# Kernel optimization log

Hardware: AMD Instinct MI355X
Metric: run time of the kernel (lower is better)

Reference implementation:

```python
import jax, jax.numpy as jnp
import numpy as np

# ProbLog program semantics, closed-form:
# Grid 2x2, cell index = 2*X + Y: 0=(0,0), 1=(0,1), 2=(1,0), 3=(1,1).
# Actions (query order): 0=stay, 1=up, 2=down, 3=left, 4=right.
# transition/5 only defines clauses for stay/up/down (plus west/east which never
# unify with left/right), so left/right can never produce 'unsafe'.
# unsafe :- pacman(X,Y), action(A), transition(X,Y,A,X1,Y1), ghost(X1,Y1).
# evidence(safe) conditions the action query: P(a|safe) = p_a(a)*safe(a)/sum.

def _build_T():
    T = np.zeros((5, 4, 4), dtype=np.float32)  # [action, pac_cell, ghost_cell]
    for c in range(4):
        T[0, c, c] = 1.0  # stay
    # up: (x,y)->(x,y+1): cell0->1, cell2->3 (y=1 cells move off-grid -> no ghost)
    T[1, 0, 1] = 1.0
    T[1, 2, 3] = 1.0
    # down: (x,y)->(x,y-1): cell1->0, cell3->2
    T[2, 1, 0] = 1.0
    T[2, 3, 2] = 1.0
    # left/right: no transition clauses -> always safe
    return T

_T = _build_T()


def setup_inputs() -> dict:
    key = jax.random.key(0)
    ks = jax.random.split(key, 4)
    B, H = 16384, 2048
    s = 1.0 / np.sqrt(H)
    return {
        "x": jax.random.normal(ks[0], (B, H), dtype=jnp.float32),
        "Wg": jax.random.normal(ks[1], (H, 4), dtype=jnp.float32) * s,
        "bg": jnp.zeros((4,), dtype=jnp.float32),
        "Wp": jax.random.normal(ks[2], (H, 4), dtype=jnp.float32) * s,
        "bp": jnp.zeros((4,), dtype=jnp.float32),
        "Wa": jax.random.normal(ks[3], (H, 5), dtype=jnp.float32) * s,
        "ba": jnp.zeros((5,), dtype=jnp.float32),
    }


def reference(x, Wg, bg, Wp, bp, Wa, ba):
    ghost = jax.nn.softmax(x @ Wg + bg, axis=-1)   # [B,4]
    pacman = jax.nn.softmax(x @ Wp + bp, axis=-1)  # [B,4]
    base = jax.nn.softmax(x @ Wa + ba, axis=-1)    # [B,5]
    T = jnp.asarray(_T)                            # [5,4,4]
    # P(unsafe | action=a) = sum_c pac[c] * ghost[target(c,a)]
    unsafe = jnp.einsum('bc,acd,bd->ba', pacman, T, ghost)  # [B,5]
    joint = base * (1.0 - unsafe)                  # P(action=a, safe)
    return joint / jnp.sum(joint, axis=-1, keepdims=True)   # P(action=a | safe)
```

## Files before the change

kernel.cpp:

```cpp
#include <hip/hip_runtime.h>
#include <hip/hip_fp16.h>


__global__ __launch_bounds__(256, 2)
void dpl_safe_policy_kernel(const float* __restrict__ x,
                            const float* __restrict__ Wg, const float* __restrict__ bg,
                            const float* __restrict__ Wp, const float* __restrict__ bp,
                            const float* __restrict__ Wa, const float* __restrict__ ba,
                            float* __restrict__ out)
{
    __shared__ __half wlds[13 * 2048];
    __shared__ float4 xt[4][2][72];

    const int tid = threadIdx.x;

    for (int idx = tid; idx < 13 * 2048; idx += 256) {
        const int j = idx >> 11, h = idx & 2047;
        float v;
        if (j < 4)      v = Wg[h * 4 + j];
        else if (j < 8) v = Wp[h * 4 + (j - 4)];
        else            v = Wa[h * 5 + (j - 8)];
        wlds[idx] = __float2half(v);
    }
    __syncthreads();

    const int w  = tid >> 6;
    const int l  = tid & 63;
    const int r8 = l & 7;
    const int p  = l >> 3;
    const int rowbase = blockIdx.x * 32 + w * 8;

    const float4* xg = (const float4*)x;
    const long gbase = (long)(rowbase + p) * 512 + r8;

    float4* tw = &xt[w][0][0];
    const int wr_off = p * 9 + r8;
    const int rd_off = r8 * 9 + p;

    float4 x0 = xg[gbase];
    tw[wr_off] = x0;
    float4 xn0 = xg[gbase + 8];
    float4 xn1 = xg[gbase + 16];
    float4 xn2 = xg[gbase + 24];

    float acc[13];
    #pragma unroll
    for (int j = 0; j < 13; ++j) acc[j] = 0.f;

    const __half2* w2 = (const __half2*)wlds;

    #pragma unroll 4
    for (int c = 0; c < 64; ++c) {
        const int buf = c & 1;
        if (c + 1 < 64) tw[(buf ^ 1) * 72 + wr_off] = xn0;
        xn0 = xn1; xn1 = xn2;
        if (c + 4 < 64) xn2 = xg[gbase + (c + 4) * 8];
        const float4 xv = tw[buf * 72 + rd_off];
        const int wb = c * 16 + p * 2;
        #pragma unroll
        for (int j = 0; j < 13; ++j) {
            const __half2 ha = w2[j * 1024 + wb];
            const __half2 hb = w2[j * 1024 + wb + 1];
            const float2 fa = __half22float2(ha);
            const float2 fb = __half22float2(hb);
            acc[j] += xv.x * fa.x + xv.y * fa.y + xv.z * fb.x + xv.w * fb.y;
        }
    }

    #pragma unroll
    for (int j = 0; j < 13; ++j) {
        acc[j] += __shfl_xor(acc[j], 8,  64);
        acc[j] += __shfl_xor(acc[j], 16, 64);
        acc[j] += __shfl_xor(acc[j], 32, 64);
    }

    const float g0 = acc[0] + bg[0], g1 = acc[1] + bg[1], g2 = acc[2] + bg[2], g3 = acc[3] + bg[3];
    const float q0 = acc[4] + bp[0], q1 = acc[5] + bp[1], q2 = acc[6] + bp[2], q3 = acc[7] + bp[3];
    const float a0 = acc[8] + ba[0], a1 = acc[9] + ba[1], a2 = acc[10] + ba[2],
                a3 = acc[11] + ba[3], a4 = acc[12] + ba[4];

    float m, s, inv;
    m = fmaxf(fmaxf(g0, g1), fmaxf(g2, g3));
    const float eg0 = __expf(g0 - m), eg1 = __expf(g1 - m), eg2 = __expf(g2 - m), eg3 = __expf(g3 - m);
    s = eg0 + eg1 + eg2 + eg3; inv = 1.f / s;
    const float G0 = eg0 * inv, G1 = eg1 * inv, G2 = eg2 * inv, G3 = eg3 * inv;

    m = fmaxf(fmaxf(q0, q1), fmaxf(q2, q3));
    const float ep0 = __expf(q0 - m), ep1 = __expf(q1 - m), ep2 = __expf(q2 - m), ep3 = __expf(q3 - m);
    s = ep0 + ep1 + ep2 + ep3; inv = 1.f / s;
    const float P0 = ep0 * inv, P1 = ep1 * inv, P2 = ep2 * inv, P3 = ep3 * inv;

    m = fmaxf(fmaxf(fmaxf(a0, a1), fmaxf(a2, a3)), a4);
    const float ea0 = __expf(a0 - m), ea1 = __expf(a1 - m), ea2 = __expf(a2 - m),
                ea3 = __expf(a3 - m), ea4 = __expf(a4 - m);
    s = ea0 + ea1 + ea2 + ea3 + ea4; inv = 1.f / s;
    const float A0 = ea0 * inv, A1 = ea1 * inv, A2 = ea2 * inv, A3 = ea3 * inv, A4 = ea4 * inv;

    const float u0 = P0 * G0 + P1 * G1 + P2 * G2 + P3 * G3;
    const float u1 = P0 * G1 + P2 * G3;
    const float u2 = P1 * G0 + P3 * G2;

    const float j0 = A0 * (1.f - u0), j1 = A1 * (1.f - u1), j2 = A2 * (1.f - u2),
                j3 = A3, j4 = A4;
    const float isd = 1.f / (j0 + j1 + j2 + j3 + j4);

    const int row = rowbase + r8;
    const float ov = (p == 0) ? j0 : (p == 1) ? j1 : (p == 2) ? j2 : (p == 3) ? j3 : j4;
    if (p < 5) out[row * 5 + p] = ov * isd;
}

extern "C" void kernel_launch(void* const* d_in, const int* in_sizes, int n_in,
                              void* d_out, int out_size, void* d_ws, size_t ws_size,
                              hipStream_t stream) {
    const float* x  = (const float*)d_in[0];
    const float* Wg = (const float*)d_in[1];
    const float* bg = (const float*)d_in[2];
    const float* Wp = (const float*)d_in[3];
    const float* bp = (const float*)d_in[4];
    const float* Wa = (const float*)d_in[5];
    const float* ba = (const float*)d_in[6];
    float* out = (float*)d_out;

    const int B = in_sizes[0] / 2048;
    const int grid = B / 32;
    dpl_safe_policy_kernel<<<grid, 256, 0, stream>>>(x, Wg, bg, Wp, bp, Wa, ba, out);
}
```

Baseline: 224.3 us.

## Restructure GEMV to two rows per lane with packed fp16 dot2 and no LDS transpose

Each lane now processes two rows over 16 H-slices, so every LDS weight load is reused for two rows. The LDS transpose buffer for x is removed in favour of direct coalesced float4 loads with a two-step register prefetch. x is converted to packed fp16 and accumulated with v_dot2 instructions. Weight staging into LDS now uses vectorized float4 reads. This cuts LDS traffic and FMA count, at the cost of quantizing x to fp16 with round-toward-zero, which could reduce accuracy, plus more accumulator registers.

```diff
diff --git a/kernel.cpp b/kernel.cpp
--- a/kernel.cpp
+++ b/kernel.cpp
@@ -1,6 +1,9 @@
 #include <hip/hip_runtime.h>
 #include <hip/hip_fp16.h>
 
+
+typedef __fp16 h2_t __attribute__((ext_vector_type(2)));
+typedef __fp16 h4_t __attribute__((ext_vector_type(4)));
 
 __global__ __launch_bounds__(256, 2)
 void dpl_safe_policy_kernel(const float* __restrict__ x,
@@ -9,104 +12,135 @@
                             const float* __restrict__ Wa, const float* __restrict__ ba,
                             float* __restrict__ out)
 {
-    __shared__ __half wlds[13 * 2048];
-    __shared__ float4 xt[4][2][72];
+    __shared__ __align__(16) __fp16 wlds[13 * 2048];
 
     const int tid = threadIdx.x;
 
-    for (int idx = tid; idx < 13 * 2048; idx += 256) {
-        const int j = idx >> 11, h = idx & 2047;
-        float v;
-        if (j < 4)      v = Wg[h * 4 + j];
-        else if (j < 8) v = Wp[h * 4 + (j - 4)];
-        else            v = Wa[h * 5 + (j - 8)];
-        wlds[idx] = __float2half(v);
+    const float4* Wg4 = (const float4*)Wg;
+    const float4* Wp4 = (const float4*)Wp;
+    for (int h = tid; h < 2048; h += 256) {
+        float4 g = Wg4[h];
+        wlds[0 * 2048 + h] = (__fp16)g.x;
+        wlds[1 * 2048 + h] = (__fp16)g.y;
+        wlds[2 * 2048 + h] = (__fp16)g.z;
+        wlds[3 * 2048 + h] = (__fp16)g.w;
+        float4 p = Wp4[h];
+        wlds[4 * 2048 + h] = (__fp16)p.x;
+        wlds[5 * 2048 + h] = (__fp16)p.y;
+        wlds[6 * 2048 + h] = (__fp16)p.z;
+        wlds[7 * 2048 + h] = (__fp16)p.w;
+        #pragma unroll
+        for (int j = 0; j < 5; ++j)
+            wlds[(8 + j) * 2048 + h] = (__fp16)Wa[h * 5 + j];
     }
     __syncthreads();
 
     const int w  = tid >> 6;
     const int l  = tid & 63;
-    const int r8 = l & 7;
-    const int p  = l >> 3;
+    const int hs = l & 15;
+    const int rg = l >> 4;
     const int rowbase = blockIdx.x * 32 + w * 8;
+    const int row0 = rowbase + rg * 2;
 
     const float4* xg = (const float4*)x;
-    const long gbase = (long)(rowbase + p) * 512 + r8;
+    const long b0 = (long)row0 * 512 + hs;
+    const long b1 = b0 + 512;
 
-    float4* tw = &xt[w][0][0];
-    const int wr_off = p * 9 + r8;
-    const int rd_off = r8 * 9 + p;
+    const h4_t* w4 = (const h4_t*)wlds;
 
-    float4 x0 = xg[gbase];
-    tw[wr_off] = x0;
-    float4 xn0 = xg[gbase + 8];
-    float4 xn1 = xg[gbase + 16];
-    float4 xn2 = xg[gbase + 24];
+    float acc0[13], acc1[13];
+    #pragma unroll
+    for (int j = 0; j < 13; ++j) { acc0[j] = 0.f; acc1[j] = 0.f; }
 
-    float acc[13];
-    #pragma unroll
-    for (int j = 0; j < 13; ++j) acc[j] = 0.f;
+    float4 c00 = xg[b0],      c10 = xg[b1];
+    float4 c01 = xg[b0 + 16], c11 = xg[b1 + 16];
 
-    const __half2* w2 = (const __half2*)wlds;
-
-    #pragma unroll 4
-    for (int c = 0; c < 64; ++c) {
-        const int buf = c & 1;
-        if (c + 1 < 64) tw[(buf ^ 1) * 72 + wr_off] = xn0;
-        xn0 = xn1; xn1 = xn2;
-        if (c + 4 < 64) xn2 = xg[gbase + (c + 4) * 8];
-        const float4 xv = tw[buf * 72 + rd_off];
-        const int wb = c * 16 + p * 2;
+    #pragma unroll 2
+    for (int c = 0; c < 32; ++c) {
+        const float4 xv0 = c00, xv1 = c10;
+        c00 = c01; c10 = c11;
+        if (c + 2 < 32) {
+            c01 = xg[b0 + (c + 2) * 16];
+            c11 = xg[b1 + (c + 2) * 16];
+        }
+        const h2_t xl0 = __builtin_amdgcn_cvt_pkrtz(xv0.x, xv0.y);
+        const h2_t xh0 = __builtin_amdgcn_cvt_pkrtz(xv0.z, xv0.w);
+        const h2_t xl1 = __builtin_amdgcn_cvt_pkrtz(xv1.x, xv1.y);
+        const h2_t xh1 = __builtin_amdgcn_cvt_pkrtz(xv1.z, xv1.w);
+        const int wb = c * 16 + hs;
         #pragma unroll
         for (int j = 0; j < 13; ++j) {
-            const __half2 ha = w2[j * 1024 + wb];
-            const __half2 hb = w2[j * 1024 + wb + 1];
-            const float2 fa = __half22float2(ha);
-            const float2 fb = __half22float2(hb);
-            acc[j] += xv.x * fa.x + xv.y * fa.y + xv.z * fb.x + xv.w * fb.y;
+            const h4_t wv = w4[j * 512 + wb];
+            const h2_t wlo = __builtin_shufflevector(wv, wv, 0, 1);
+            const h2_t whi = __builtin_shufflevector(wv, wv, 2, 3);
+#if __has_builtin(__builtin_amdgcn_fdot2)
+            acc0[j] = __builtin_amdgcn_fdot2(xl0, wlo, acc0[j], false);
+            acc0[j] = __builtin_amdgcn_fdot2(xh0, whi, acc0[j], false);
+            acc1[j] = __builtin_amdgcn_fdot2(xl1, wlo, acc1[j], false);
+            acc1[j] = __builtin_amdgcn_fdot2(xh1, whi, acc1[j], false);
+#else
+            acc0[j] += (float)xl0.x * (float)wlo.x + (float)xl0.y * (float)wlo.y
+                     + (float)xh0.x * (float)whi.x + (float)xh0.y * (float)whi.y;
+            acc1[j] += (float)xl1.x * (float)wlo.x + (float)xl1.y * (float)wlo.y
+                     + (float)xh1.x * (float)whi.x + (float)xh1.y * (float)whi.y;
+#endif
         }
     }
 
     #pragma unroll
     for (int j = 0; j < 13; ++j) {
-        acc[j] += __shfl_xor(acc[j], 8,  64);
-        acc[j] += __shfl_xor(acc[j], 16, 64);
-        acc[j] += __shfl_xor(acc[j], 32, 64);
+        acc0[j] += __shfl_xor(acc0[j], 1, 64);
+        acc0[j] += __shfl_xor(acc0[j], 2, 64);
+        acc0[j] += __shfl_xor(acc0[j], 4, 64);
+        acc0[j] += __shfl_xor(acc0[j], 8, 64);
+        acc1[j] += __shfl_xor(acc1[j], 1, 64);
+        acc1[j] += __shfl_xor(acc1[j], 2, 64);
+        acc1[j] += __shfl_xor(acc1[j], 4, 64);
+        acc1[j] += __shfl_xor(acc1[j], 8, 64);
     }
 
-    const float g0 = acc[0] + bg[0], g1 = acc[1] + bg[1], g2 = acc[2] + bg[2], g3 = acc[3] + bg[3];
-    const float q0 = acc[4] + bp[0], q1 = acc[5] + bp[1], q2 = acc[6] + bp[2], q3 = acc[7] + bp[3];
-    const float a0 = acc[8] + ba[0], a1 = acc[9] + ba[1], a2 = acc[10] + ba[2],
-                a3 = acc[11] + ba[3], a4 = acc[12] + ba[4];
+    const float vbg0 = bg[0], vbg1 = bg[1], vbg2 = bg[2], vbg3 = bg[3];
+    const float vbp0 = bp[0], vbp1 = bp[1], vbp2 = bp[2], vbp3 = bp[3];
+    const float vba0 = ba[0], vba1 = ba[1], vba2 = ba[2], vba3 = ba[3], vba4 = ba[4];
 
-    float m, s, inv;
-    m = fmaxf(fmaxf(g0, g1), fmaxf(g2, g3));
-    const float eg0 = __expf(g0 - m), eg1 = __expf(g1 - m), eg2 = __expf(g2 - m), eg3 = __expf(g3 - m);
-    s = eg0 + eg1 + eg2 + eg3; inv = 1.f / s;
-    const float G0 = eg0 * inv, G1 = eg1 * inv, G2 = eg2 * inv, G3 = eg3 * inv;
+    #pragma unroll
+    for (int r = 0; r < 2; ++r) {
+        const float* acc = r ? acc1 : acc0;
+        const float g0 = acc[0] + vbg0, g1 = acc[1] + vbg1, g2 = acc[2] + vbg2, g3 = acc[3] + vbg3;
+        const float q0 = acc[4] + vbp0, q1 = acc[5] + vbp1, q2 = acc[6] + vbp2, q3 = acc[7] + vbp3;
+        const float a0 = acc[8] + vba0, a1 = acc[9] + vba1, a2 = acc[10] + vba2,
+                    a3 = acc[11] + vba3, a4 = acc[12] + vba4;
 
-    m = fmaxf(fmaxf(q0, q1), fmaxf(q2, q3));
-    const float ep0 = __expf(q0 - m), ep1 = __expf(q1 - m), ep2 = __expf(q2 - m), ep3 = __expf(q3 - m);
-    s = ep0 + ep1 + ep2 + ep3; inv = 1.f / s;
-    const float P0 = ep0 * inv, P1 = ep1 * inv, P2 = ep2 * inv, P3 = ep3 * inv;
+        float m, s, inv;
+        m = fmaxf(fmaxf(g0, g1), fmaxf(g2, g3));
+        const float eg0 = __expf(g0 - m), eg1 = __expf(g1 - m), eg2 = __expf(g2 - m), eg3 = __expf(g3 - m);
+        s = eg0 + eg1 + eg2 + eg3; inv = 1.f / s;
+        const float G0 = eg0 * inv, G1 = eg1 * inv, G2 = eg2 * inv, G3 = eg3 * inv;
 
-    m = fmaxf(fmaxf(fmaxf(a0, a1), fmaxf(a2, a3)), a4);
-    const float ea0 = __expf(a0 - m), ea1 = __expf(a1 - m), ea2 = __expf(a2 - m),
-                ea3 = __expf(a3 - m), ea4 = __expf(a4 - m);
-    s = ea0 + ea1 + ea2 + ea3 + ea4; inv = 1.f / s;
-    const float A0 = ea0 * inv, A1 = ea1 * inv, A2 = ea2 * inv, A3 = ea3 * inv, A4 = ea4 * inv;
+        m = fmaxf(fmaxf(q0, q1), fmaxf(q2, q3));
+        const float ep0 = __expf(q0 - m), ep1 = __expf(q1 - m), ep2 = __expf(q2 - m), ep3 = __expf(q3 - m);
+        s = ep0 + ep1 + ep2 + ep3; inv = 1.f / s;
+        const float P0 = ep0 * inv, P1 = ep1 * inv, P2 = ep2 * inv, P3 = ep3 * inv;
 
-    const float u0 = P0 * G0 + P1 * G1 + P2 * G2 + P3 * G3;
-    const float u1 = P0 * G1 + P2 * G3;
-    const float u2 = P1 * G0 + P3 * G2;
+        m = fmaxf(fmaxf(fmaxf(a0, a1), fmaxf(a2, a3)), a4);
+        const float ea0 = __expf(a0 - m), ea1 = __expf(a1 - m), ea2 = __expf(a2 - m),
+                    ea3 = __expf(a3 - m), ea4 = __expf(a4 - m);
+        s = ea0 + ea1 + ea2 + ea3 + ea4; inv = 1.f / s;
+        const float A0 = ea0 * inv, A1 = ea1 * inv, A2 = ea2 * inv, A3 = ea3 * inv, A4 = ea4 * inv;
 
-    const float j0 = A0 * (1.f - u0), j1 = A1 * (1.f - u1), j2 = A2 * (1.f - u2),
-                j3 = A3, j4 = A4;
-    const float isd = 1.f / (j0 + j1 + j2 + j3 + j4);
+        const float u0 = P0 * G0 + P1 * G1 + P2 * G2 + P3 * G3;
+        const float u1 = P0 * G1 + P2 * G3;
+        const float u2 = P1 * G0 + P3 * G2;
 
-    const int row = rowbase + r8;
-    const float ov = (p == 0) ? j0 : (p == 1) ? j1 : (p == 2) ? j2 : (p == 3) ? j3 : j4;
-    if (p < 5) out[row * 5 + p] = ov * isd;
+        const float j0 = A0 * (1.f - u0), j1 = A1 * (1.f - u1), j2 = A2 * (1.f - u2),
+                    j3 = A3, j4 = A4;
+        const float isd = 1.f / (j0 + j1 + j2 + j3 + j4);
+
+        if (hs < 5) {
+            const float ov = (hs == 0) ? j0 : (hs == 1) ? j1 : (hs == 2) ? j2 : (hs == 3) ? j3 : j4;
+            out[(row0 + r) * 5 + hs] = ov * isd;
+        }
+    }
 }
 
 extern "C" void kernel_launch(void* const* d_in, const int* in_sizes, int n_in,
```

Result: faster. 210.2 us (-6.3%).

## Replace scalar FMA dot products with fp16 MFMA using prepacked weight fragments

Applied to the files above, without the earlier changes.

Adds a small pre-kernel that converts the concatenated weights to fp16 and packs them into MFMA B-fragment order in workspace. The main kernel converts x tiles to fp16 in registers and runs 16x16x32 MFMAs, with each block's K dimension split across wave pairs and the partial sums combined through shared memory. This removes the per-block LDS weight staging and the scalar FMA loop. It costs an extra kernel launch, rounds x to fp16, and uses hardcoded grid sizes.

```diff
diff --git a/kernel.cpp b/kernel.cpp
--- a/kernel.cpp
+++ b/kernel.cpp
@@ -1,112 +1,129 @@
 #include <hip/hip_runtime.h>
-#include <hip/hip_fp16.h>
 
 
+typedef __fp16 h2_t __attribute__((ext_vector_type(2)));
+typedef __fp16 h4_t __attribute__((ext_vector_type(4)));
+typedef __fp16 h8_t __attribute__((ext_vector_type(8)));
+typedef float f32x4 __attribute__((ext_vector_type(4)));
+
+__global__ void pack_bfrag(const float* __restrict__ Wg,
+                           const float* __restrict__ Wp,
+                           const float* __restrict__ Wa,
+                           h8_t* __restrict__ bfrag)
+{
+    const int t = blockIdx.x * 256 + threadIdx.x;
+    const int iter = t >> 6, lane = t & 63;
+    const int n = lane & 15, kg = lane >> 4;
+    h8_t v;
+    #pragma unroll
+    for (int j = 0; j < 8; ++j) {
+        const int k = iter * 32 + kg * 8 + j;
+        float f;
+        if (n < 4)       f = Wg[k * 4 + n];
+        else if (n < 8)  f = Wp[k * 4 + (n - 4)];
+        else if (n < 13) f = Wa[k * 5 + (n - 8)];
+        else             f = 0.f;
+        v[j] = (__fp16)f;
+    }
+    bfrag[t] = v;
+}
+
 __global__ __launch_bounds__(256, 2)
-void dpl_safe_policy_kernel(const float* __restrict__ x,
-                            const float* __restrict__ Wg, const float* __restrict__ bg,
-                            const float* __restrict__ Wp, const float* __restrict__ bp,
-                            const float* __restrict__ Wa, const float* __restrict__ ba,
-                            float* __restrict__ out)
+void gemm_mfma(const float* __restrict__ x,
+               const h8_t* __restrict__ bfrag,
+               const float* __restrict__ bg, const float* __restrict__ bp,
+               const float* __restrict__ ba, float* __restrict__ out)
 {
-    __shared__ __half wlds[13 * 2048];
-    __shared__ float4 xt[4][2][72];
+    __shared__ float dt[2][2][16][17];
 
     const int tid = threadIdx.x;
-
-    for (int idx = tid; idx < 13 * 2048; idx += 256) {
-        const int j = idx >> 11, h = idx & 2047;
-        float v;
-        if (j < 4)      v = Wg[h * 4 + j];
-        else if (j < 8) v = Wp[h * 4 + (j - 4)];
-        else            v = Wa[h * 5 + (j - 8)];
-        wlds[idx] = __float2half(v);
-    }
-    __syncthreads();
-
-    const int w  = tid >> 6;
-    const int l  = tid & 63;
-    const int r8 = l & 7;
-    const int p  = l >> 3;
-    const int rowbase = blockIdx.x * 32 + w * 8;
+    const int w   = tid >> 6;
+    const int l   = tid & 63;
+    const int rt2 = w & 1;
+    const int ks  = w >> 1;
+    const int row0 = blockIdx.x * 32 + rt2 * 16;
+    const int m  = l & 15;
+    const int kg = l >> 4;
 
     const float4* xg = (const float4*)x;
-    const long gbase = (long)(rowbase + p) * 512 + r8;
+    const long base = (long)(row0 + m) * 512 + ks * 256 + kg * 2;
+    const h8_t* bf = bfrag + (ks * 32) * 64 + l;
 
-    float4* tw = &xt[w][0][0];
-    const int wr_off = p * 9 + r8;
-    const int rd_off = r8 * 9 + p;
+    float4 pa[4], pb[4];
+    h8_t   pf[4];
+    #pragma unroll
+    for (int d = 0; d < 4; ++d) {
+        pa[d] = xg[base + d * 8];
+        pb[d] = xg[base + d * 8 + 1];
+        pf[d] = bf[d * 64];
+    }
 
-    float4 x0 = xg[gbase];
-    tw[wr_off] = x0;
-    float4 xn0 = xg[gbase + 8];
-    float4 xn1 = xg[gbase + 16];
-    float4 xn2 = xg[gbase + 24];
-
-    float acc[13];
-    #pragma unroll
-    for (int j = 0; j < 13; ++j) acc[j] = 0.f;
-
-    const __half2* w2 = (const __half2*)wlds;
+    f32x4 acc = {0.f, 0.f, 0.f, 0.f};
 
     #pragma unroll 4
-    for (int c = 0; c < 64; ++c) {
-        const int buf = c & 1;
-        if (c + 1 < 64) tw[(buf ^ 1) * 72 + wr_off] = xn0;
-        xn0 = xn1; xn1 = xn2;
-        if (c + 4 < 64) xn2 = xg[gbase + (c + 4) * 8];
-        const float4 xv = tw[buf * 72 + rd_off];
-        const int wb = c * 16 + p * 2;
-        #pragma unroll
-        for (int j = 0; j < 13; ++j) {
-            const __half2 ha = w2[j * 1024 + wb];
-            const __half2 hb = w2[j * 1024 + wb + 1];
-            const float2 fa = __half22float2(ha);
-            const float2 fb = __half22float2(hb);
-            acc[j] += xv.x * fa.x + xv.y * fa.y + xv.z * fb.x + xv.w * fb.y;
+    for (int i = 0; i < 32; ++i) {
+        const int s = i & 3;
+        const float4 xa = pa[s], xb = pb[s];
+        const h8_t b8 = pf[s];
+        if (i + 4 < 32) {
+            pa[s] = xg[base + (i + 4) * 8];
+            pb[s] = xg[base + (i + 4) * 8 + 1];
+            pf[s] = bf[(i + 4) * 64];
         }
+        const h2_t a01 = __builtin_amdgcn_cvt_pkrtz(xa.x, xa.y);
+        const h2_t a23 = __builtin_amdgcn_cvt_pkrtz(xa.z, xa.w);
+        const h2_t a45 = __builtin_amdgcn_cvt_pkrtz(xb.x, xb.y);
+        const h2_t a67 = __builtin_amdgcn_cvt_pkrtz(xb.z, xb.w);
+        const h4_t alo = __builtin_shufflevector(a01, a23, 0, 1, 2, 3);
+        const h4_t ahi = __builtin_shufflevector(a45, a67, 0, 1, 2, 3);
+        const h8_t a8  = __builtin_shufflevector(alo, ahi, 0, 1, 2, 3, 4, 5, 6, 7);
+        acc = __builtin_amdgcn_mfma_f32_16x16x32_f16(a8, b8, acc, 0, 0, 0);
     }
 
     #pragma unroll
-    for (int j = 0; j < 13; ++j) {
-        acc[j] += __shfl_xor(acc[j], 8,  64);
-        acc[j] += __shfl_xor(acc[j], 16, 64);
-        acc[j] += __shfl_xor(acc[j], 32, 64);
+    for (int r = 0; r < 4; ++r)
+        dt[rt2][ks][kg * 4 + r][m] = acc[r];
+    __syncthreads();
+
+    if (w < 2 && l < 16) {
+        float lg[13];
+        #pragma unroll
+        for (int c = 0; c < 13; ++c)
+            lg[c] = dt[w][0][l][c] + dt[w][1][l][c];
+
+        const float g0 = lg[0] + bg[0], g1 = lg[1] + bg[1], g2 = lg[2] + bg[2], g3 = lg[3] + bg[3];
+        const float q0 = lg[4] + bp[0], q1 = lg[5] + bp[1], q2 = lg[6] + bp[2], q3 = lg[7] + bp[3];
+        const float a0 = lg[8] + ba[0], a1 = lg[9] + ba[1], a2 = lg[10] + ba[2],
+                    a3 = lg[11] + ba[3], a4 = lg[12] + ba[4];
+
+        float mx, sum, inv;
+        mx = fmaxf(fmaxf(g0, g1), fmaxf(g2, g3));
+        const float eg0 = __expf(g0 - mx), eg1 = __expf(g1 - mx), eg2 = __expf(g2 - mx), eg3 = __expf(g3 - mx);
+        sum = eg0 + eg1 + eg2 + eg3; inv = 1.f / sum;
+        const float G0 = eg0 * inv, G1 = eg1 * inv, G2 = eg2 * inv, G3 = eg3 * inv;
+
+        mx = fmaxf(fmaxf(q0, q1), fmaxf(q2, q3));
+        const float ep0 = __expf(q0 - mx), ep1 = __expf(q1 - mx), ep2 = __expf(q2 - mx), ep3 = __expf(q3 - mx);
+        sum = ep0 + ep1 + ep2 + ep3; inv = 1.f / sum;
+        const float P0 = ep0 * inv, P1 = ep1 * inv, P2 = ep2 * inv, P3 = ep3 * inv;
+
+        mx = fmaxf(fmaxf(fmaxf(a0, a1), fmaxf(a2, a3)), a4);
+        const float ea0 = __expf(a0 - mx), ea1 = __expf(a1 - mx), ea2 = __expf(a2 - mx),
+                    ea3 = __expf(a3 - mx), ea4 = __expf(a4 - mx);
+        sum = ea0 + ea1 + ea2 + ea3 + ea4; inv = 1.f / sum;
+        const float A0 = ea0 * inv, A1 = ea1 * inv, A2 = ea2 * inv, A3 = ea3 * inv, A4 = ea4 * inv;
+
+        const float u0 = P0 * G0 + P1 * G1 + P2 * G2 + P3 * G3;
+        const float u1 = P0 * G1 + P2 * G3;
+        const float u2 = P1 * G0 + P3 * G2;
+
+        const float j0 = A0 * (1.f - u0), j1 = A1 * (1.f - u1), j2 = A2 * (1.f - u2),
+                    j3 = A3, j4 = A4;
+        const float isd = 1.f / (j0 + j1 + j2 + j3 + j4);
+
+        float* o = out + (long)(row0 + l) * 5;
+        o[0] = j0 * isd; o[1] = j1 * isd; o[2] = j2 * isd; o[3] = j3 * isd; o[4] = j4 * isd;
     }
-
-    const float g0 = acc[0] + bg[0], g1 = acc[1] + bg[1], g2 = acc[2] + bg[2], g3 = acc[3] + bg[3];
-    const float q0 = acc[4] + bp[0], q1 = acc[5] + bp[1], q2 = acc[6] + bp[2], q3 = acc[7] + bp[3];
-    const float a0 = acc[8] + ba[0], a1 = acc[9] + ba[1], a2 = acc[10] + ba[2],
-                a3 = acc[11] + ba[3], a4 = acc[12] + ba[4];
-
-    float m, s, inv;
-    m = fmaxf(fmaxf(g0, g1), fmaxf(g2, g3));
-    const float eg0 = __expf(g0 - m), eg1 = __expf(g1 - m), eg2 = __expf(g2 - m), eg3 = __expf(g3 - m);
-    s = eg0 + eg1 + eg2 + eg3; inv = 1.f / s;
-    const float G0 = eg0 * inv, G1 = eg1 * inv, G2 = eg2 * inv, G3 = eg3 * inv;
-
-    m = fmaxf(fmaxf(q0, q1), fmaxf(q2, q3));
-    const float ep0 = __expf(q0 - m), ep1 = __expf(q1 - m), ep2 = __expf(q2 - m), ep3 = __expf(q3 - m);
-    s = ep0 + ep1 + ep2 + ep3; inv = 1.f / s;
-    const float P0 = ep0 * inv, P1 = ep1 * inv, P2 = ep2 * inv, P3 = ep3 * inv;
-
-    m = fmaxf(fmaxf(fmaxf(a0, a1), fmaxf(a2, a3)), a4);
-    const float ea0 = __expf(a0 - m), ea1 = __expf(a1 - m), ea2 = __expf(a2 - m),
-                ea3 = __expf(a3 - m), ea4 = __expf(a4 - m);
-    s = ea0 + ea1 + ea2 + ea3 + ea4; inv = 1.f / s;
-    const float A0 = ea0 * inv, A1 = ea1 * inv, A2 = ea2 * inv, A3 = ea3 * inv, A4 = ea4 * inv;
-
-    const float u0 = P0 * G0 + P1 * G1 + P2 * G2 + P3 * G3;
-    const float u1 = P0 * G1 + P2 * G3;
-    const float u2 = P1 * G0 + P3 * G2;
-
-    const float j0 = A0 * (1.f - u0), j1 = A1 * (1.f - u1), j2 = A2 * (1.f - u2),
-                j3 = A3, j4 = A4;
-    const float isd = 1.f / (j0 + j1 + j2 + j3 + j4);
-
-    const int row = rowbase + r8;
-    const float ov = (p == 0) ? j0 : (p == 1) ? j1 : (p == 2) ? j2 : (p == 3) ? j3 : j4;
-    if (p < 5) out[row * 5 + p] = ov * isd;
 }
 
 extern "C" void kernel_launch(void* const* d_in, const int* in_sizes, int n_in,
@@ -121,7 +138,8 @@
     const float* ba = (const float*)d_in[6];
     float* out = (float*)d_out;
 
-    const int B = in_sizes[0] / 2048;
-    const int grid = B / 32;
-    dpl_safe_policy_kernel<<<grid, 256, 0, stream>>>(x, Wg, bg, Wp, bp, Wa, ba, out);
+    h8_t* bfrag = (h8_t*)d_ws;
+
+    pack_bfrag<<<16, 256, 0, stream>>>(Wg, Wp, Wa, bfrag);
+    gemm_mfma<<<512, 256, 0, stream>>>(x, bfrag, bg, bp, ba, out);
 }
```

After: 208.0 us. -7.3%, faster.
